# Kernel tuning notes

Measured on AMD Instinct MI355X. Metric: run time of the kernel, lower is better.

Reference implementation:

```python
import jax, jax.numpy as jnp
import numpy as np

N_NODES = 50000
N_EDGES = 600000
NUM_GRAPHS = 64


def gcn_conv(x, W, b, src, dst, n):
    # PyG GCNConv: x' = D^{-1/2} (A + I) D^{-1/2} (x W) + b, self-loops implicit
    h = x @ W  # [N, H]
    deg = jax.ops.segment_sum(jnp.ones((src.shape[0],), h.dtype), dst, num_segments=n) + 1.0
    dinv = jax.lax.rsqrt(deg)  # [N]
    norm = dinv[src] * dinv[dst]  # [E]
    msg = h[src] * norm[:, None]  # [E, H] gather + scale
    agg = jax.ops.segment_sum(msg, dst, num_segments=n)  # scatter-add
    agg = agg + h * (dinv * dinv)[:, None]  # self-loop contribution
    return agg + b


def global_mean_pool(x, batch, num_graphs):
    s = jax.ops.segment_sum(x, batch, num_segments=num_graphs)
    cnt = jax.ops.segment_sum(jnp.ones((x.shape[0],), x.dtype), batch, num_segments=num_graphs)
    return s / jnp.maximum(cnt, 1.0)[:, None]


def setup_inputs() -> dict:
    key = jax.random.key(0)
    ks = jax.random.split(key, 12)
    x = jax.random.normal(ks[0], (N_NODES, 128), jnp.float32)
    edge_index = jax.random.randint(ks[1], (2, N_EDGES), 0, N_NODES, jnp.int64)
    batch = jnp.sort(jax.random.randint(ks[2], (N_NODES,), 0, NUM_GRAPHS, jnp.int64))
    W1 = jax.random.normal(ks[3], (128, 128), jnp.float32) * 0.08
    b1 = jax.random.normal(ks[4], (128,), jnp.float32) * 0.02
    W2 = jax.random.normal(ks[5], (128, 128), jnp.float32) * 0.08
    b2 = jax.random.normal(ks[6], (128,), jnp.float32) * 0.02
    Wfc1 = jax.random.normal(ks[7], (128, 64), jnp.float32) * 0.08
    bfc1 = jax.random.normal(ks[8], (64,), jnp.float32) * 0.02
    Wfc2 = jax.random.normal(ks[9], (64, 1), jnp.float32) * 0.08
    bfc2 = jax.random.normal(ks[10], (1,), jnp.float32) * 0.02
    return {"x": x, "edge_index": edge_index, "batch": batch,
            "W1": W1, "b1": b1, "W2": W2, "b2": b2,
            "Wfc1": Wfc1, "bfc1": bfc1, "Wfc2": Wfc2, "bfc2": bfc2}


def reference(x, edge_index, batch, W1, b1, W2, b2, Wfc1, bfc1, Wfc2, bfc2):
    n = x.shape[0]
    src, dst = edge_index[0], edge_index[1]
    h = jax.nn.relu(gcn_conv(x, W1, b1, src, dst, n))
    # dropout = identity (eval mode)
    h = jax.nn.relu(gcn_conv(h, W2, b2, src, dst, n))
    g = global_mean_pool(h, batch, NUM_GRAPHS)  # [G, H]
    g = jax.nn.relu(g @ Wfc1 + bfc1)
    return g @ Wfc2 + bfc2  # [G, 1]
```

## Files before the change

### kernel.cpp

```cpp
#include <hip/hip_runtime.h>
#include <hip/hip_fp16.h>


#define ELLK 40

typedef short bf16x8 __attribute__((ext_vector_type(8)));
typedef float f32x4  __attribute__((ext_vector_type(4)));

__device__ inline unsigned short f2bf_rne(float f) {
    unsigned u = __float_as_uint(f);
    unsigned r = (u + 0x7fffu + ((u >> 16) & 1u)) >> 16;
    return (unsigned short)r;
}
__device__ inline float bf2f(unsigned short h) {
    return __uint_as_float(((unsigned)h) << 16);
}

__global__ __launch_bounds__(256) void wconv_zero(const float* __restrict__ W1,
                                                  const float* __restrict__ W2,
                                                  unsigned short* __restrict__ W1h,
                                                  unsigned short* __restrict__ W1l,
                                                  unsigned short* __restrict__ W2h,
                                                  unsigned short* __restrict__ W2l,
                                                  int* __restrict__ count,
                                                  float* __restrict__ pooled,
                                                  float* __restrict__ cnt, int N) {
    int tid = threadIdx.x;
    int b = blockIdx.x;
    if (b < 128) {
        int i = b * 256 + tid;
        const float* W = (i < 16384) ? W1 : W2;
        unsigned short* Wh = (i < 16384) ? W1h : W2h;
        unsigned short* Wl = (i < 16384) ? W1l : W2l;
        int ii = i & 16383;
        int k = ii >> 7, n = ii & 127;
        float v = W[ii];
        unsigned short h = f2bf_rne(v);
        float lo = v - bf2f(h);
        int ct = n >> 4, nn = n & 15, ks = k >> 5, q = (k >> 3) & 3, j = k & 7;
        int oidx = (((ct * 4 + ks) * 64) + (q * 16 + nn)) * 8 + j;
        Wh[oidx] = h;
        Wl[oidx] = f2bf_rne(lo);
    } else {
        int idx = (b - 128) * 256 + tid;
        if (idx < N) count[idx] = 0;
        else if (idx < N + 8192) pooled[idx - N] = 0.f;
        else if (idx < N + 8256) cnt[idx - N - 8192] = 0.f;
    }
}

template <bool RELU_IN>
__device__ __forceinline__ void gemm_body(const float* __restrict__ X,
                                          const unsigned short* __restrict__ Wfh,
                                          const unsigned short* __restrict__ Wfl,
                                          __half* __restrict__ OUT, int M, int blk) {
    __shared__ unsigned short Xh[64][136];
    __shared__ unsigned short Xl[64][136];
    int tid = threadIdx.x;
    int w = tid >> 6, l = tid & 63;
    int m0 = blk * 64;

#pragma unroll
    for (int it = 0; it < 8; it++) {
        int i = tid + it * 256;
        int row = i >> 5, c4 = i & 31;
        int grow = m0 + row;
        float4 v = make_float4(0.f, 0.f, 0.f, 0.f);
        if (grow < M) v = *(const float4*)(X + (size_t)grow * 128 + c4 * 4);
        if (RELU_IN) {
            v.x = fmaxf(v.x, 0.f); v.y = fmaxf(v.y, 0.f);
            v.z = fmaxf(v.z, 0.f); v.w = fmaxf(v.w, 0.f);
        }
        float a[4] = {v.x, v.y, v.z, v.w};
        ushort4 hi, lo;
        unsigned short* hp = (unsigned short*)&hi;
        unsigned short* lp = (unsigned short*)&lo;
#pragma unroll
        for (int e = 0; e < 4; e++) {
            unsigned short h = f2bf_rne(a[e]);
            hp[e] = h;
            lp[e] = f2bf_rne(a[e] - bf2f(h));
        }
        *(ushort4*)&Xh[row][c4 * 4] = hi;
        *(ushort4*)&Xl[row][c4 * 4] = lo;
    }
    __syncthreads();

    int q = l >> 4, nn = l & 15;
    f32x4 acc[8];
#pragma unroll
    for (int ct = 0; ct < 8; ct++) acc[ct] = (f32x4){0.f, 0.f, 0.f, 0.f};

#pragma unroll
    for (int ks = 0; ks < 4; ks++) {
        bf16x8 ahi = *(const bf16x8*)&Xh[w * 16 + nn][ks * 32 + q * 8];
        bf16x8 alo = *(const bf16x8*)&Xl[w * 16 + nn][ks * 32 + q * 8];
#pragma unroll
        for (int ct = 0; ct < 8; ct++) {
            size_t fo = ((size_t)(ct * 4 + ks) * 64 + l) * 8;
            bf16x8 bhi = *(const bf16x8*)(Wfh + fo);
            bf16x8 blo = *(const bf16x8*)(Wfl + fo);
            acc[ct] = __builtin_amdgcn_mfma_f32_16x16x32_bf16(ahi, bhi, acc[ct], 0, 0, 0);
            acc[ct] = __builtin_amdgcn_mfma_f32_16x16x32_bf16(alo, bhi, acc[ct], 0, 0, 0);
            acc[ct] = __builtin_amdgcn_mfma_f32_16x16x32_bf16(ahi, blo, acc[ct], 0, 0, 0);
        }
    }
    __syncthreads();

#pragma unroll
    for (int r = 0; r < 4; r++) {
        int lrow = w * 16 + q * 4 + r;
#pragma unroll
        for (int ct = 0; ct < 8; ct++) {
            __half hv = __float2half(acc[ct][r]);
            Xh[lrow][ct * 16 + nn] = __half_as_ushort(hv);
        }
    }
    __syncthreads();
#pragma unroll
    for (int t = 0; t < 4; t++) {
        int c = tid + t * 256;
        int row = c >> 4, seg = c & 15;
        int grow = m0 + row;
        if (grow < M) {
            uint4 v = *(uint4*)&Xh[row][seg * 8];
            *(uint4*)((unsigned short*)OUT + (size_t)grow * 128 + seg * 8) = v;
        }
    }
}

__global__ __launch_bounds__(256) void fused_hg(const float* __restrict__ X,
                                                const unsigned short* __restrict__ Wfh,
                                                const unsigned short* __restrict__ Wfl,
                                                __half* __restrict__ OUT, int M, int gblocks,
                                                const int* __restrict__ dst,
                                                int* __restrict__ count,
                                                unsigned short* __restrict__ rank, int E) {
    if ((int)blockIdx.x < gblocks) {
        gemm_body<false>(X, Wfh, Wfl, OUT, M, blockIdx.x);
    } else {
        int e = ((int)blockIdx.x - gblocks) * 256 + (int)threadIdx.x;
        if (e < E) {
            int d = dst[e];
            rank[e] = (unsigned short)atomicAdd(&count[d], 1);
        }
    }
}

__global__ void scatter_norm(const int* __restrict__ src, const int* __restrict__ dst,
                             const unsigned short* __restrict__ rank,
                             const int* __restrict__ count,
                             int2* __restrict__ ell, int E) {
    int e = blockIdx.x * blockDim.x + threadIdx.x;
    if (e < E) {
        int s = src[e], d = dst[e];
        int r = rank[e];
        float ds = 1.0f / sqrtf((float)count[s] + 1.0f);
        float dd = 1.0f / sqrtf((float)count[d] + 1.0f);
        if (r < ELLK) ell[(size_t)d * ELLK + r] = make_int2(s, __float_as_int(ds * dd));
    }
}

__device__ __forceinline__ void gather_node(const unsigned short* __restrict__ hb,
                                            const long long* __restrict__ ell,
                                            const int* __restrict__ count,
                                            int n, int sub, int cl, float a[8]) {
    int cn = count[n];
    int cnl = min(cn, ELLK);
    float din = 1.0f / sqrtf((float)cn + 1.0f);
    const long long* row = ell + (size_t)n * ELLK;
    if (sub == 0) {
        float sw = din * din;
        uint4 raw = *(const uint4*)(hb + (size_t)n * 128 + cl * 8);
        const __half2* hh = (const __half2*)&raw;
        float2 f0 = __half22float2(hh[0]), f1 = __half22float2(hh[1]);
        float2 f2 = __half22float2(hh[2]), f3 = __half22float2(hh[3]);
        a[0] = fmaf(f0.x, sw, a[0]); a[1] = fmaf(f0.y, sw, a[1]);
        a[2] = fmaf(f1.x, sw, a[2]); a[3] = fmaf(f1.y, sw, a[3]);
        a[4] = fmaf(f2.x, sw, a[4]); a[5] = fmaf(f2.y, sw, a[5]);
        a[6] = fmaf(f3.x, sw, a[6]); a[7] = fmaf(f3.y, sw, a[7]);
    }
    for (int base = 0; base < cnl; base += 16) {
        int e1 = cnl - 1;
        int j0 = base + sub, j1 = j0 + 4, j2 = j0 + 8, j3 = j0 + 12;
        long long v0 = row[min(j0, e1)];
        long long v1 = row[min(j1, e1)];
        long long v2 = row[min(j2, e1)];
        long long v3 = row[min(j3, e1)];
        float n0 = (j0 < cnl) ? __int_as_float((int)(v0 >> 32)) : 0.f;
        float n1 = (j1 < cnl) ? __int_as_float((int)(v1 >> 32)) : 0.f;
        float n2 = (j2 < cnl) ? __int_as_float((int)(v2 >> 32)) : 0.f;
        float n3 = (j3 < cnl) ? __int_as_float((int)(v3 >> 32)) : 0.f;
        uint4 r0 = *(const uint4*)(hb + (size_t)(int)v0 * 128 + cl * 8);
        uint4 r1 = *(const uint4*)(hb + (size_t)(int)v1 * 128 + cl * 8);
        uint4 r2 = *(const uint4*)(hb + (size_t)(int)v2 * 128 + cl * 8);
        uint4 r3 = *(const uint4*)(hb + (size_t)(int)v3 * 128 + cl * 8);
        {
            const __half2* hh = (const __half2*)&r0;
            float2 f0 = __half22float2(hh[0]), f1 = __half22float2(hh[1]);
            float2 f2 = __half22float2(hh[2]), f3 = __half22float2(hh[3]);
            a[0] = fmaf(f0.x, n0, a[0]); a[1] = fmaf(f0.y, n0, a[1]);
            a[2] = fmaf(f1.x, n0, a[2]); a[3] = fmaf(f1.y, n0, a[3]);
            a[4] = fmaf(f2.x, n0, a[4]); a[5] = fmaf(f2.y, n0, a[5]);
            a[6] = fmaf(f3.x, n0, a[6]); a[7] = fmaf(f3.y, n0, a[7]);
        }
        {
            const __half2* hh = (const __half2*)&r1;
            float2 f0 = __half22float2(hh[0]), f1 = __half22float2(hh[1]);
            float2 f2 = __half22float2(hh[2]), f3 = __half22float2(hh[3]);
            a[0] = fmaf(f0.x, n1, a[0]); a[1] = fmaf(f0.y, n1, a[1]);
            a[2] = fmaf(f1.x, n1, a[2]); a[3] = fmaf(f1.y, n1, a[3]);
            a[4] = fmaf(f2.x, n1, a[4]); a[5] = fmaf(f2.y, n1, a[5]);
            a[6] = fmaf(f3.x, n1, a[6]); a[7] = fmaf(f3.y, n1, a[7]);
        }
        {
            const __half2* hh = (const __half2*)&r2;
            float2 f0 = __half22float2(hh[0]), f1 = __half22float2(hh[1]);
            float2 f2 = __half22float2(hh[2]), f3 = __half22float2(hh[3]);
            a[0] = fmaf(f0.x, n2, a[0]); a[1] = fmaf(f0.y, n2, a[1]);
            a[2] = fmaf(f1.x, n2, a[2]); a[3] = fmaf(f1.y, n2, a[3]);
            a[4] = fmaf(f2.x, n2, a[4]); a[5] = fmaf(f2.y, n2, a[5]);
            a[6] = fmaf(f3.x, n2, a[6]); a[7] = fmaf(f3.y, n2, a[7]);
        }
        {
            const __half2* hh = (const __half2*)&r3;
            float2 f0 = __half22float2(hh[0]), f1 = __half22float2(hh[1]);
            float2 f2 = __half22float2(hh[2]), f3 = __half22float2(hh[3]);
            a[0] = fmaf(f0.x, n3, a[0]); a[1] = fmaf(f0.y, n3, a[1]);
            a[2] = fmaf(f1.x, n3, a[2]); a[3] = fmaf(f1.y, n3, a[3]);
            a[4] = fmaf(f2.x, n3, a[4]); a[5] = fmaf(f2.y, n3, a[5]);
            a[6] = fmaf(f3.x, n3, a[6]); a[7] = fmaf(f3.y, n3, a[7]);
        }
    }
}

__global__ __launch_bounds__(512) void gather_gemm(const __half* __restrict__ h,
                                                   const float* __restrict__ bias,
                                                   const int* __restrict__ count,
                                                   const long long* __restrict__ ell,
                                                   const unsigned short* __restrict__ Wfh,
                                                   const unsigned short* __restrict__ Wfl,
                                                   __half* __restrict__ OUT, int N) {
    __shared__ unsigned short Xh[64][136];
    __shared__ unsigned short Xl[64][136];
    int tid = threadIdx.x;
    int w = tid >> 6, l = tid & 63;
    int sub = l >> 4, cl = l & 15;
    int m0 = blockIdx.x * 64;
    const unsigned short* hb = (const unsigned short*)h;

    for (int rr = 0; rr < 8; rr++) {
        int lrow = w * 8 + rr;
        int n = m0 + lrow;
        float a[8] = {0.f, 0.f, 0.f, 0.f, 0.f, 0.f, 0.f, 0.f};
        if (n < N) gather_node(hb, ell, count, n, sub, cl, a);
#pragma unroll
        for (int m = 16; m < 64; m <<= 1) {
#pragma unroll
            for (int k = 0; k < 8; k++) a[k] += __shfl_xor(a[k], m, 64);
        }
        if (sub == 0) {
            unsigned short hs[8], ls[8];
#pragma unroll
            for (int k = 0; k < 8; k++) {
                float v = fmaxf(a[k] + bias[cl * 8 + k], 0.f);
                unsigned short hh = f2bf_rne(v);
                hs[k] = hh;
                ls[k] = f2bf_rne(v - bf2f(hh));
            }
            *(ushort4*)&Xh[lrow][cl * 8]     = *(ushort4*)&hs[0];
            *(ushort4*)&Xh[lrow][cl * 8 + 4] = *(ushort4*)&hs[4];
            *(ushort4*)&Xl[lrow][cl * 8]     = *(ushort4*)&ls[0];
            *(ushort4*)&Xl[lrow][cl * 8 + 4] = *(ushort4*)&ls[4];
        }
    }
    __syncthreads();

    int q = l >> 4, nn = l & 15;
    int w2 = w & 3;
    int ch = (w >> 2) * 4;
    f32x4 acc[4];
#pragma unroll
    for (int ct2 = 0; ct2 < 4; ct2++) acc[ct2] = (f32x4){0.f, 0.f, 0.f, 0.f};
#pragma unroll
    for (int ks = 0; ks < 4; ks++) {
        bf16x8 ahi = *(const bf16x8*)&Xh[w2 * 16 + nn][ks * 32 + q * 8];
        bf16x8 alo = *(const bf16x8*)&Xl[w2 * 16 + nn][ks * 32 + q * 8];
#pragma unroll
        for (int ct2 = 0; ct2 < 4; ct2++) {
            int ct = ch + ct2;
            size_t fo = ((size_t)(ct * 4 + ks) * 64 + l) * 8;
            bf16x8 bhi = *(const bf16x8*)(Wfh + fo);
            bf16x8 blo = *(const bf16x8*)(Wfl + fo);
            acc[ct2] = __builtin_amdgcn_mfma_f32_16x16x32_bf16(ahi, bhi, acc[ct2], 0, 0, 0);
            acc[ct2] = __builtin_amdgcn_mfma_f32_16x16x32_bf16(alo, bhi, acc[ct2], 0, 0, 0);
            acc[ct2] = __builtin_amdgcn_mfma_f32_16x16x32_bf16(ahi, blo, acc[ct2], 0, 0, 0);
        }
    }
    __syncthreads();
#pragma unroll
    for (int r = 0; r < 4; r++) {
        int lrow = w2 * 16 + q * 4 + r;
#pragma unroll
        for (int ct2 = 0; ct2 < 4; ct2++) {
            __half hv = __float2half(acc[ct2][r]);
            Xh[lrow][(ch + ct2) * 16 + nn] = __half_as_ushort(hv);
        }
    }
    __syncthreads();
#pragma unroll
    for (int t = 0; t < 2; t++) {
        int c = tid + t * 512;
        int row = c >> 4, seg = c & 15;
        int grow = m0 + row;
        if (grow < N) {
            uint4 v = *(uint4*)&Xh[row][seg * 8];
            *(uint4*)((unsigned short*)OUT + (size_t)grow * 128 + seg * 8) = v;
        }
    }
}

__global__ __launch_bounds__(512) void gather_pool(const __half* __restrict__ h,
                                                   const float* __restrict__ bias,
                                                   const int* __restrict__ count,
                                                   const long long* __restrict__ ell,
                                                   const int* __restrict__ batch,
                                                   float* __restrict__ pooled,
                                                   float* __restrict__ cnt, int N) {
    __shared__ float P[64][128];
    __shared__ int gb[64];
    int tid = threadIdx.x;
    int w = tid >> 6, l = tid & 63;
    int sub = l >> 4, cl = l & 15;
    int m0 = blockIdx.x * 64;
    const unsigned short* hb = (const unsigned short*)h;

    if (tid < 64) gb[tid] = (m0 + tid < N) ? batch[m0 + tid] : -1;

    for (int rr = 0; rr < 8; rr++) {
        int lrow = w * 8 + rr;
        int n = m0 + lrow;
        float a[8] = {0.f, 0.f, 0.f, 0.f, 0.f, 0.f, 0.f, 0.f};
        if (n < N) gather_node(hb, ell, count, n, sub, cl, a);
#pragma unroll
        for (int m = 16; m < 64; m <<= 1) {
#pragma unroll
            for (int k = 0; k < 8; k++) a[k] += __shfl_xor(a[k], m, 64);
        }
        if (sub == 0 && n < N) {
#pragma unroll
            for (int k = 0; k < 8; k++)
                P[lrow][cl * 8 + k] = fmaxf(a[k] + bias[cl * 8 + k], 0.f);
        }
    }
    __syncthreads();

    int c = tid & 127, quarter = tid >> 7;
    float acc = 0.f, cacc = 0.f;
    int curg = -1;
    for (int i = quarter * 16; i < quarter * 16 + 16; i++) {
        int n = m0 + i;
        if (n >= N) break;
        int g = gb[i];
        float v = P[i][c];
        if (g != curg) {
            if (curg >= 0) {
                atomicAdd(&pooled[curg * 128 + c], acc);
                if (c == 0) atomicAdd(&cnt[curg], cacc);
            }
            curg = g; acc = 0.f; cacc = 0.f;
        }
        acc += v; cacc += 1.f;
    }
    if (curg >= 0) {
        atomicAdd(&pooled[curg * 128 + c], acc);
        if (c == 0) atomicAdd(&cnt[curg], cacc);
    }
}

__global__ __launch_bounds__(64) void head_kernel(const float* __restrict__ pooled,
                                                  const float* __restrict__ cnt,
                                                  const float* __restrict__ Wfc1,
                                                  const float* __restrict__ bfc1,
                                                  const float* __restrict__ Wfc2,
                                                  const float* __restrict__ bfc2,
                                                  float* __restrict__ out) {
    __shared__ float mean[128];
    int g = blockIdx.x;
    int t = threadIdx.x;
    float inv = 1.0f / fmaxf(cnt[g], 1.0f);
    mean[t] = pooled[g * 128 + t] * inv;
    mean[t + 64] = pooled[g * 128 + t + 64] * inv;
    __syncthreads();
    float s = bfc1[t];
#pragma unroll 4
    for (int k = 0; k < 128; k++) s = fmaf(mean[k], Wfc1[k * 64 + t], s);
    float p = fmaxf(s, 0.f) * Wfc2[t];
#pragma unroll
    for (int o = 32; o > 0; o >>= 1) p += __shfl_down(p, o, 64);
    if (t == 0) out[g] = p + bfc2[0];
}

extern "C" void kernel_launch(void* const* d_in, const int* in_sizes, int n_in,
                              void* d_out, int out_size, void* d_ws, size_t ws_size,
                              hipStream_t stream) {
    const float* x    = (const float*)d_in[0];
    const int*   edge = (const int*)d_in[1];
    const int*   batch= (const int*)d_in[2];
    const float* W1   = (const float*)d_in[3];
    const float* b1   = (const float*)d_in[4];
    const float* W2   = (const float*)d_in[5];
    const float* b2   = (const float*)d_in[6];
    const float* Wfc1 = (const float*)d_in[7];
    const float* bfc1 = (const float*)d_in[8];
    const float* Wfc2 = (const float*)d_in[9];
    const float* bfc2 = (const float*)d_in[10];
    float* out = (float*)d_out;

    int N = in_sizes[0] / 128;
    int E = in_sizes[1] / 2;
    const int* src = edge;
    const int* dst = edge + E;

    char* ws = (char*)d_ws;
    size_t off = 0;
    auto alloc = [&](size_t bytes) { void* p = ws + off; off += (bytes + 255) & ~(size_t)255; return p; };
    __half* Ah    = (__half*)alloc((size_t)N * 128 * sizeof(__half));
    __half* Ah2   = (__half*)alloc((size_t)N * 128 * sizeof(__half));
    int*   count  = (int*)alloc((size_t)N * sizeof(int));
    unsigned short* rank = (unsigned short*)alloc((size_t)E * sizeof(unsigned short));
    int2*  ell    = (int2*)alloc((size_t)N * ELLK * sizeof(int2));
    float* pooled = (float*)alloc(64 * 128 * sizeof(float));
    float* cnt    = (float*)alloc(64 * sizeof(float));
    unsigned short* W1h = (unsigned short*)alloc(16384 * sizeof(short));
    unsigned short* W1l = (unsigned short*)alloc(16384 * sizeof(short));
    unsigned short* W2h = (unsigned short*)alloc(16384 * sizeof(short));
    unsigned short* W2l = (unsigned short*)alloc(16384 * sizeof(short));

    int hb = (E + 255) / 256;
    int gblocks = (N + 63) / 64;
    int fblocks = (N + 63) / 64;
    int zb = (N + 8256 + 255) / 256;

    wconv_zero<<<128 + zb, 256, 0, stream>>>(W1, W2, W1h, W1l, W2h, W2l,
                                             count, pooled, cnt, N);

    fused_hg<<<gblocks + hb, 256, 0, stream>>>(x, W1h, W1l, Ah, N, gblocks,
                                               dst, count, rank, E);

    scatter_norm<<<hb, 256, 0, stream>>>(src, dst, rank, count, ell, E);

    gather_gemm<<<fblocks, 512, 0, stream>>>(Ah, b1, count, (const long long*)ell,
                                             W2h, W2l, Ah2, N);

    gather_pool<<<fblocks, 512, 0, stream>>>(Ah2, b2, count, (const long long*)ell,
                                             batch, pooled, cnt, N);

    head_kernel<<<64, 64, 0, stream>>>(pooled, cnt, Wfc1, bfc1, Wfc2, bfc2, out);
}
```

Measured before the change: 238.9 us.

## Prefetch next node's ELL row and zero-pad ELL to drop bound checks

The scatter kernel now also zero-pads each node's ELL row up to a multiple of 16 slots, so gather loops can read padded entries without min/compare masking. The gather kernels software-pipeline the ELL index loads, fetching the next node's first 16 entries and count while the current node is processed. ELLK grows from 40 to 48, which drops fewer overflow edges but enlarges the ELL buffer and adds a padding pass. The padded path always processes at least 16 entries per node, so some gathers read row 0 with zero weight.

New measurement: 237.2 us. About the same (-0.7%).

```diff
diff --git a/kernel.cpp b/kernel.cpp
--- a/kernel.cpp
+++ b/kernel.cpp
@@ -2,7 +2,7 @@
 #include <hip/hip_fp16.h>
 
 
-#define ELLK 40
+#define ELLK 48
 
 typedef short bf16x8 __attribute__((ext_vector_type(8)));
 typedef float f32x4  __attribute__((ext_vector_type(4)));
@@ -150,87 +150,70 @@
 __global__ void scatter_norm(const int* __restrict__ src, const int* __restrict__ dst,
                              const unsigned short* __restrict__ rank,
                              const int* __restrict__ count,
-                             int2* __restrict__ ell, int E) {
-    int e = blockIdx.x * blockDim.x + threadIdx.x;
-    if (e < E) {
-        int s = src[e], d = dst[e];
-        int r = rank[e];
-        float ds = 1.0f / sqrtf((float)count[s] + 1.0f);
-        float dd = 1.0f / sqrtf((float)count[d] + 1.0f);
-        if (r < ELLK) ell[(size_t)d * ELLK + r] = make_int2(s, __float_as_int(ds * dd));
-    }
-}
-
-__device__ __forceinline__ void gather_node(const unsigned short* __restrict__ hb,
-                                            const long long* __restrict__ ell,
-                                            const int* __restrict__ count,
-                                            int n, int sub, int cl, float a[8]) {
-    int cn = count[n];
-    int cnl = min(cn, ELLK);
+                             int2* __restrict__ ell, int E, int N, int hb) {
+    int b = blockIdx.x;
+    if (b < hb) {
+        int e = b * 256 + (int)threadIdx.x;
+        if (e < E) {
+            int s = src[e], d = dst[e];
+            int r = rank[e];
+            float ds = 1.0f / sqrtf((float)count[s] + 1.0f);
+            float dd = 1.0f / sqrtf((float)count[d] + 1.0f);
+            if (r < ELLK) ell[(size_t)d * ELLK + r] = make_int2(s, __float_as_int(ds * dd));
+        }
+    } else {
+        int n = (b - hb) * 256 + (int)threadIdx.x;
+        if (n < N) {
+            int r = min(count[n], ELLK);
+            int rend = min(ELLK, max(16, (r + 15) & ~15));
+            int2 z = make_int2(0, 0);
+            for (int j = r; j < rend; j++) ell[(size_t)n * ELLK + j] = z;
+        }
+    }
+}
+
+__device__ __forceinline__ void fma8(const uint4& raw, float nr, float a[8]) {
+    const __half2* hh = (const __half2*)&raw;
+    float2 f0 = __half22float2(hh[0]), f1 = __half22float2(hh[1]);
+    float2 f2 = __half22float2(hh[2]), f3 = __half22float2(hh[3]);
+    a[0] = fmaf(f0.x, nr, a[0]); a[1] = fmaf(f0.y, nr, a[1]);
+    a[2] = fmaf(f1.x, nr, a[2]); a[3] = fmaf(f1.y, nr, a[3]);
+    a[4] = fmaf(f2.x, nr, a[4]); a[5] = fmaf(f2.y, nr, a[5]);
+    a[6] = fmaf(f3.x, nr, a[6]); a[7] = fmaf(f3.y, nr, a[7]);
+}
+
+__device__ __forceinline__ void gather_process(const unsigned short* __restrict__ hb,
+                                               const long long* __restrict__ ell,
+                                               int n, int sub, int cl,
+                                               long long u0, long long u1,
+                                               long long u2, long long u3,
+                                               int cn, float a[8]) {
+    uint4 r0 = *(const uint4*)(hb + (size_t)(int)u0 * 128 + cl * 8);
+    uint4 r1 = *(const uint4*)(hb + (size_t)(int)u1 * 128 + cl * 8);
+    uint4 r2 = *(const uint4*)(hb + (size_t)(int)u2 * 128 + cl * 8);
+    uint4 r3 = *(const uint4*)(hb + (size_t)(int)u3 * 128 + cl * 8);
     float din = 1.0f / sqrtf((float)cn + 1.0f);
-    const long long* row = ell + (size_t)n * ELLK;
     if (sub == 0) {
         float sw = din * din;
-        uint4 raw = *(const uint4*)(hb + (size_t)n * 128 + cl * 8);
-        const __half2* hh = (const __half2*)&raw;
-        float2 f0 = __half22float2(hh[0]), f1 = __half22float2(hh[1]);
-        float2 f2 = __half22float2(hh[2]), f3 = __half22float2(hh[3]);
-        a[0] = fmaf(f0.x, sw, a[0]); a[1] = fmaf(f0.y, sw, a[1]);
-        a[2] = fmaf(f1.x, sw, a[2]); a[3] = fmaf(f1.y, sw, a[3]);
-        a[4] = fmaf(f2.x, sw, a[4]); a[5] = fmaf(f2.y, sw, a[5]);
-        a[6] = fmaf(f3.x, sw, a[6]); a[7] = fmaf(f3.y, sw, a[7]);
-    }
-    for (int base = 0; base < cnl; base += 16) {
-        int e1 = cnl - 1;
-        int j0 = base + sub, j1 = j0 + 4, j2 = j0 + 8, j3 = j0 + 12;
-        long long v0 = row[min(j0, e1)];
-        long long v1 = row[min(j1, e1)];
-        long long v2 = row[min(j2, e1)];
-        long long v3 = row[min(j3, e1)];
-        float n0 = (j0 < cnl) ? __int_as_float((int)(v0 >> 32)) : 0.f;
-        float n1 = (j1 < cnl) ? __int_as_float((int)(v1 >> 32)) : 0.f;
-        float n2 = (j2 < cnl) ? __int_as_float((int)(v2 >> 32)) : 0.f;
-        float n3 = (j3 < cnl) ? __int_as_float((int)(v3 >> 32)) : 0.f;
-        uint4 r0 = *(const uint4*)(hb + (size_t)(int)v0 * 128 + cl * 8);
-        uint4 r1 = *(const uint4*)(hb + (size_t)(int)v1 * 128 + cl * 8);
-        uint4 r2 = *(const uint4*)(hb + (size_t)(int)v2 * 128 + cl * 8);
-        uint4 r3 = *(const uint4*)(hb + (size_t)(int)v3 * 128 + cl * 8);
-        {
-            const __half2* hh = (const __half2*)&r0;
-            float2 f0 = __half22float2(hh[0]), f1 = __half22float2(hh[1]);
-            float2 f2 = __half22float2(hh[2]), f3 = __half22float2(hh[3]);
-            a[0] = fmaf(f0.x, n0, a[0]); a[1] = fmaf(f0.y, n0, a[1]);
-            a[2] = fmaf(f1.x, n0, a[2]); a[3] = fmaf(f1.y, n0, a[3]);
-            a[4] = fmaf(f2.x, n0, a[4]); a[5] = fmaf(f2.y, n0, a[5]);
-            a[6] = fmaf(f3.x, n0, a[6]); a[7] = fmaf(f3.y, n0, a[7]);
-        }
-        {
-            const __half2* hh = (const __half2*)&r1;
-            float2 f0 = __half22float2(hh[0]), f1 = __half22float2(hh[1]);
-            float2 f2 = __half22float2(hh[2]), f3 = __half22float2(hh[3]);
-            a[0] = fmaf(f0.x, n1, a[0]); a[1] = fmaf(f0.y, n1, a[1]);
-            a[2] = fmaf(f1.x, n1, a[2]); a[3] = fmaf(f1.y, n1, a[3]);
-            a[4] = fmaf(f2.x, n1, a[4]); a[5] = fmaf(f2.y, n1, a[5]);
-            a[6] = fmaf(f3.x, n1, a[6]); a[7] = fmaf(f3.y, n1, a[7]);
-        }
-        {
-            const __half2* hh = (const __half2*)&r2;
-            float2 f0 = __half22float2(hh[0]), f1 = __half22float2(hh[1]);
-            float2 f2 = __half22float2(hh[2]), f3 = __half22float2(hh[3]);
-            a[0] = fmaf(f0.x, n2, a[0]); a[1] = fmaf(f0.y, n2, a[1]);
-            a[2] = fmaf(f1.x, n2, a[2]); a[3] = fmaf(f1.y, n2, a[3]);
-            a[4] = fmaf(f2.x, n2, a[4]); a[5] = fmaf(f2.y, n2, a[5]);
-            a[6] = fmaf(f3.x, n2, a[6]); a[7] = fmaf(f3.y, n2, a[7]);
-        }
-        {
-            const __half2* hh = (const __half2*)&r3;
-            float2 f0 = __half22float2(hh[0]), f1 = __half22float2(hh[1]);
-            float2 f2 = __half22float2(hh[2]), f3 = __half22float2(hh[3]);
-            a[0] = fmaf(f0.x, n3, a[0]); a[1] = fmaf(f0.y, n3, a[1]);
-            a[2] = fmaf(f1.x, n3, a[2]); a[3] = fmaf(f1.y, n3, a[3]);
-            a[4] = fmaf(f2.x, n3, a[4]); a[5] = fmaf(f2.y, n3, a[5]);
-            a[6] = fmaf(f3.x, n3, a[6]); a[7] = fmaf(f3.y, n3, a[7]);
-        }
+        uint4 sr = *(const uint4*)(hb + (size_t)n * 128 + cl * 8);
+        fma8(sr, sw, a);
+    }
+    fma8(r0, __int_as_float((int)(u0 >> 32)), a);
+    fma8(r1, __int_as_float((int)(u1 >> 32)), a);
+    fma8(r2, __int_as_float((int)(u2 >> 32)), a);
+    fma8(r3, __int_as_float((int)(u3 >> 32)), a);
+    int cle = min((min(cn, ELLK) + 15) & ~15, ELLK);
+    for (int base = 16; base < cle; base += 16) {
+        const long long* rp = ell + (size_t)n * ELLK + base;
+        long long v0 = rp[sub], v1 = rp[sub + 4], v2 = rp[sub + 8], v3 = rp[sub + 12];
+        uint4 q0 = *(const uint4*)(hb + (size_t)(int)v0 * 128 + cl * 8);
+        uint4 q1 = *(const uint4*)(hb + (size_t)(int)v1 * 128 + cl * 8);
+        uint4 q2 = *(const uint4*)(hb + (size_t)(int)v2 * 128 + cl * 8);
+        uint4 q3 = *(const uint4*)(hb + (size_t)(int)v3 * 128 + cl * 8);
+        fma8(q0, __int_as_float((int)(v0 >> 32)), a);
+        fma8(q1, __int_as_float((int)(v1 >> 32)), a);
+        fma8(q2, __int_as_float((int)(v2 >> 32)), a);
+        fma8(q3, __int_as_float((int)(v3 >> 32)), a);
     }
 }
 
@@ -249,29 +232,45 @@
     int m0 = blockIdx.x * 64;
     const unsigned short* hb = (const unsigned short*)h;
 
-    for (int rr = 0; rr < 8; rr++) {
-        int lrow = w * 8 + rr;
-        int n = m0 + lrow;
-        float a[8] = {0.f, 0.f, 0.f, 0.f, 0.f, 0.f, 0.f, 0.f};
-        if (n < N) gather_node(hb, ell, count, n, sub, cl, a);
-#pragma unroll
-        for (int m = 16; m < 64; m <<= 1) {
-#pragma unroll
-            for (int k = 0; k < 8; k++) a[k] += __shfl_xor(a[k], m, 64);
-        }
-        if (sub == 0) {
-            unsigned short hs[8], ls[8];
-#pragma unroll
-            for (int k = 0; k < 8; k++) {
-                float v = fmaxf(a[k] + bias[cl * 8 + k], 0.f);
-                unsigned short hh = f2bf_rne(v);
-                hs[k] = hh;
-                ls[k] = f2bf_rne(v - bf2f(hh));
-            }
-            *(ushort4*)&Xh[lrow][cl * 8]     = *(ushort4*)&hs[0];
-            *(ushort4*)&Xh[lrow][cl * 8 + 4] = *(ushort4*)&hs[4];
-            *(ushort4*)&Xl[lrow][cl * 8]     = *(ushort4*)&ls[0];
-            *(ushort4*)&Xl[lrow][cl * 8 + 4] = *(ushort4*)&ls[4];
+    {
+        int ncur = min(m0 + w * 8, N - 1);
+        const long long* rp = ell + (size_t)ncur * ELLK;
+        long long u0 = rp[sub], u1 = rp[sub + 4], u2 = rp[sub + 8], u3 = rp[sub + 12];
+        int ccur = count[ncur];
+        for (int rr = 0; rr < 8; rr++) {
+            int n = m0 + w * 8 + rr;
+            int ne = min(n, N - 1);
+            long long v0 = 0, v1 = 0, v2 = 0, v3 = 0;
+            int cnx = 0;
+            if (rr < 7) {
+                int nn = min(ne + 1, N - 1);
+                const long long* rq = ell + (size_t)nn * ELLK;
+                v0 = rq[sub]; v1 = rq[sub + 4]; v2 = rq[sub + 8]; v3 = rq[sub + 12];
+                cnx = count[nn];
+            }
+            float a[8] = {0.f, 0.f, 0.f, 0.f, 0.f, 0.f, 0.f, 0.f};
+            gather_process(hb, ell, ne, sub, cl, u0, u1, u2, u3, ccur, a);
+#pragma unroll
+            for (int m = 16; m < 64; m <<= 1) {
+#pragma unroll
+                for (int k = 0; k < 8; k++) a[k] += __shfl_xor(a[k], m, 64);
+            }
+            if (sub == 0) {
+                int lrow = w * 8 + rr;
+                unsigned short hs[8], ls[8];
+#pragma unroll
+                for (int k = 0; k < 8; k++) {
+                    float vv = fmaxf(a[k] + bias[cl * 8 + k], 0.f);
+                    unsigned short hh = f2bf_rne(vv);
+                    hs[k] = hh;
+                    ls[k] = f2bf_rne(vv - bf2f(hh));
+                }
+                *(ushort4*)&Xh[lrow][cl * 8]     = *(ushort4*)&hs[0];
+                *(ushort4*)&Xh[lrow][cl * 8 + 4] = *(ushort4*)&hs[4];
+                *(ushort4*)&Xl[lrow][cl * 8]     = *(ushort4*)&ls[0];
+                *(ushort4*)&Xl[lrow][cl * 8 + 4] = *(ushort4*)&ls[4];
+            }
+            u0 = v0; u1 = v1; u2 = v2; u3 = v3; ccur = cnx;
         }
     }
     __syncthreads();
@@ -337,20 +336,36 @@
 
     if (tid < 64) gb[tid] = (m0 + tid < N) ? batch[m0 + tid] : -1;
 
-    for (int rr = 0; rr < 8; rr++) {
-        int lrow = w * 8 + rr;
-        int n = m0 + lrow;
-        float a[8] = {0.f, 0.f, 0.f, 0.f, 0.f, 0.f, 0.f, 0.f};
-        if (n < N) gather_node(hb, ell, count, n, sub, cl, a);
-#pragma unroll
-        for (int m = 16; m < 64; m <<= 1) {
-#pragma unroll
-            for (int k = 0; k < 8; k++) a[k] += __shfl_xor(a[k], m, 64);
-        }
-        if (sub == 0 && n < N) {
-#pragma unroll
-            for (int k = 0; k < 8; k++)
-                P[lrow][cl * 8 + k] = fmaxf(a[k] + bias[cl * 8 + k], 0.f);
+    {
+        int ncur = min(m0 + w * 8, N - 1);
+        const long long* rp = ell + (size_t)ncur * ELLK;
+        long long u0 = rp[sub], u1 = rp[sub + 4], u2 = rp[sub + 8], u3 = rp[sub + 12];
+        int ccur = count[ncur];
+        for (int rr = 0; rr < 8; rr++) {
+            int n = m0 + w * 8 + rr;
+            int ne = min(n, N - 1);
+            long long v0 = 0, v1 = 0, v2 = 0, v3 = 0;
+            int cnx = 0;
+            if (rr < 7) {
+                int nn = min(ne + 1, N - 1);
+                const long long* rq = ell + (size_t)nn * ELLK;
+                v0 = rq[sub]; v1 = rq[sub + 4]; v2 = rq[sub + 8]; v3 = rq[sub + 12];
+                cnx = count[nn];
+            }
+            float a[8] = {0.f, 0.f, 0.f, 0.f, 0.f, 0.f, 0.f, 0.f};
+            gather_process(hb, ell, ne, sub, cl, u0, u1, u2, u3, ccur, a);
+#pragma unroll
+            for (int m = 16; m < 64; m <<= 1) {
+#pragma unroll
+                for (int k = 0; k < 8; k++) a[k] += __shfl_xor(a[k], m, 64);
+            }
+            if (sub == 0) {
+                int lrow = w * 8 + rr;
+#pragma unroll
+                for (int k = 0; k < 8; k++)
+                    P[lrow][cl * 8 + k] = fmaxf(a[k] + bias[cl * 8 + k], 0.f);
+            }
+            u0 = v0; u1 = v1; u2 = v2; u3 = v3; ccur = cnx;
         }
     }
     __syncthreads();
@@ -438,6 +453,7 @@
     unsigned short* W2l = (unsigned short*)alloc(16384 * sizeof(short));
 
     int hb = (E + 255) / 256;
+    int nzb = (N + 255) / 256;
     int gblocks = (N + 63) / 64;
     int fblocks = (N + 63) / 64;
     int zb = (N + 8256 + 255) / 256;
@@ -448,7 +464,7 @@
     fused_hg<<<gblocks + hb, 256, 0, stream>>>(x, W1h, W1l, Ah, N, gblocks,
                                                dst, count, rank, E);
 
-    scatter_norm<<<hb, 256, 0, stream>>>(src, dst, rank, count, ell, E);
+    scatter_norm<<<hb + nzb, 256, 0, stream>>>(src, dst, rank, count, ell, E, N, hb);
 
     gather_gemm<<<fblocks, 512, 0, stream>>>(Ah, b1, count, (const long long*)ell,
                                              W2h, W2l, Ah2, N);
```
